# Kernel tuning notes

Measured on AMD Instinct MI355X. Metric: run time of the kernel, lower is better.

## Reference

```python
import jax, jax.numpy as jnp
import numpy as np

N_NODES = 100000
N_EDGES = 1600000
D_IN = 64
D_OUT = 64
EDGE_DIM = 16


def setup_inputs() -> dict:
    key = jax.random.key(0)
    ks = jax.random.split(key, 6)
    x = jax.random.normal(ks[0], (N_NODES, D_IN), dtype=jnp.float32)
    edge_index = jax.random.randint(ks[1], (2, N_EDGES), 0, N_NODES, dtype=jnp.int64)
    edge_feature = jax.random.normal(ks[2], (N_EDGES, EDGE_DIM), dtype=jnp.float32)
    W_edge = jax.random.normal(ks[3], (EDGE_DIM, 1), dtype=jnp.float32) * (1.0 / np.sqrt(EDGE_DIM))
    b_edge = jnp.zeros((1,), dtype=jnp.float32)
    W_node = jax.random.normal(ks[4], (D_OUT, D_IN), dtype=jnp.float32) * (1.0 / np.sqrt(D_IN))
    b_node = jnp.zeros((D_OUT,), dtype=jnp.float32)
    return {"x": x, "edge_index": edge_index, "edge_feature": edge_feature,
            "W_edge": W_edge, "b_edge": b_edge, "W_node": W_node, "b_node": b_node}


def reference(x, edge_index, edge_feature, W_edge, b_edge, W_node, b_node):
    # per-edge gate: Linear(edge_dim -> 1) + Sigmoid  -> [E]
    gate = jax.nn.sigmoid(edge_feature @ W_edge + b_edge)[:, 0]
    # node projection: Linear(in -> out)  -> [N, D_OUT]
    xp = x @ W_node.T + b_node
    row = edge_index[0]  # destination (SparseTensor row)
    col = edge_index[1]  # source gathered
    num_nodes = x.shape[0]
    # weighted gather of source node features  -> [E, D_OUT]
    msg = gate[:, None] * xp[col]
    summed = jax.ops.segment_sum(msg, row, num_segments=num_nodes)
    cnt = jax.ops.segment_sum(jnp.ones((row.shape[0],), dtype=xp.dtype), row,
                              num_segments=num_nodes)
    # reduce='mean': divide by row nnz count; empty rows stay 0
    out = summed / jnp.maximum(cnt, 1.0)[:, None]
    return out
```

## Files before the change

kernel.cpp:

```cpp
#include <hip/hip_runtime.h>
#include <math.h>

#define NN 100000
#define NE 1600000
#define DD 64
#define ED 16
#define BROWS 192
#define NBIN 521
#define NBIN_PAD 544
#define BCAP 3840
#define EPB 4096
#define NBLKA ((NE + EPB - 1) / EPB)


__device__ __forceinline__ unsigned short f2bf(float f) {
    unsigned int b = __float_as_uint(f);
    unsigned int r = (b + 0x7FFFu + ((b >> 16) & 1u)) >> 16;
    return (unsigned short)r;
}

__global__ __launch_bounds__(256) void proj_kernel(
    const float* __restrict__ x, const float* __restrict__ Wn,
    const float* __restrict__ bn, unsigned short* __restrict__ xpb,
    int* __restrict__ cursor) {
    __shared__ float4 xs[64 * 16];
    int tid = threadIdx.x;
    if (blockIdx.x == 0) {
        cursor[tid] = tid * BCAP;
        cursor[tid + 256] = (tid + 256) * BCAP;
        if (tid < NBIN_PAD - 512) cursor[tid + 512] = (tid + 512) * BCAP;
    }
    int o = tid & 63;
    int wave = tid >> 6;
    float4 Wr[16];
    const float4* Wn4 = reinterpret_cast<const float4*>(Wn);
#pragma unroll
    for (int k = 0; k < 16; ++k) Wr[k] = Wn4[o * 16 + k];
    float bo = bn[o];
    int n0 = blockIdx.x * 64;
    const float4* x4 = reinterpret_cast<const float4*>(x);
    long base = (long)n0 * 16;
    long limit = (long)NN * 16;
#pragma unroll
    for (int i = 0; i < 4; ++i) {
        long idx = base + tid + 256 * i;
        xs[tid + 256 * i] = (idx < limit) ? x4[idx] : make_float4(0.f, 0.f, 0.f, 0.f);
    }
    __syncthreads();
#pragma unroll
    for (int j = 0; j < 16; ++j) {
        int ln = wave * 16 + j;
        int n = n0 + ln;
        if (n >= NN) break;
        float acc = bo;
#pragma unroll
        for (int k = 0; k < 16; ++k) {
            float4 a = xs[ln * 16 + k];
            acc += a.x * Wr[k].x + a.y * Wr[k].y + a.z * Wr[k].z + a.w * Wr[k].w;
        }
        xpb[(long)n * DD + o] = f2bf(acc);
    }
}

__global__ __launch_bounds__(1024) void binA_kernel(
    const int* __restrict__ ei, const float* __restrict__ ef,
    const float* __restrict__ We, const float* __restrict__ be,
    int* __restrict__ cursor, int2* __restrict__ binned) {
    __shared__ int cnt[NBIN_PAD];
    __shared__ int base[NBIN_PAD];
    int tid = threadIdx.x;
    int e0 = blockIdx.x * EPB;
    if (tid < NBIN_PAD) cnt[tid] = 0;
    __syncthreads();
    int rows[4], cols[4];
#pragma unroll
    for (int i = 0; i < 4; ++i) {
        int e = e0 + tid + 1024 * i;
        bool ok = e < NE;
        rows[i] = ok ? ei[e] : -1;
        cols[i] = ok ? ei[NE + e] : 0;
        if (ok) atomicAdd(&cnt[rows[i] / BROWS], 1);
    }
    __syncthreads();
    if (tid < NBIN_PAD) {
        int c = cnt[tid];
        base[tid] = c ? atomicAdd(&cursor[tid], c) : 0;
    }
    __syncthreads();
    if (tid < NBIN_PAD) cnt[tid] = 0;
    __syncthreads();
    const float4* We4 = reinterpret_cast<const float4*>(We);
    float4 w0 = We4[0], w1 = We4[1], w2 = We4[2], w3 = We4[3];
    float bb = be[0];
#pragma unroll
    for (int i = 0; i < 4; ++i) {
        int e = e0 + tid + 1024 * i;
        if (e < NE) {
            const float4* ef4 = reinterpret_cast<const float4*>(ef + (size_t)e * ED);
            float4 a0 = ef4[0], a1 = ef4[1], a2 = ef4[2], a3 = ef4[3];
            float d = a0.x * w0.x + a0.y * w0.y + a0.z * w0.z + a0.w * w0.w
                    + a1.x * w1.x + a1.y * w1.y + a1.z * w1.z + a1.w * w1.w
                    + a2.x * w2.x + a2.y * w2.y + a2.z * w2.z + a2.w * w2.w
                    + a3.x * w3.x + a3.y * w3.y + a3.z * w3.z + a3.w * w3.w + bb;
            float g = 1.f / (1.f + expf(-d));
            int r = rows[i], c = cols[i];
            int bin = r / BROWS;
            int rl = r - bin * BROWS;
            int pos = base[bin] + atomicAdd(&cnt[bin], 1);
            binned[pos] = make_int2((rl << 24) | c, __float_as_int(g));
        }
    }
}

__global__ __launch_bounds__(512) void binB_kernel(
    const unsigned short* __restrict__ xpb, const int* __restrict__ cursor,
    const int2* __restrict__ binned, float* __restrict__ out) {
    __shared__ int2 sorted[BCAP];
    __shared__ int hist[256];
    __shared__ int offs[256];
    __shared__ int claim[BROWS];
    int tid = threadIdx.x;
    int b = blockIdx.x;
    if (tid < 256) { hist[tid] = 0; offs[tid] = 0; }
    if (tid < BROWS) claim[tid] = 0;
    __syncthreads();
    int bstart = b * BCAP;
    int nb = cursor[b] - bstart;
    for (int t = tid; t < nb; t += 512) {
        int w = binned[bstart + t].x;
        atomicAdd(&hist[(w >> 24) & 0xFF], 1);
    }
    __syncthreads();
    if (tid < 256) offs[tid] = hist[tid];
    __syncthreads();
    for (int d = 1; d < 256; d <<= 1) {
        int add = 0;
        if (tid < 256 && tid >= d) add = offs[tid - d];
        __syncthreads();
        if (tid < 256) offs[tid] += add;
        __syncthreads();
    }
    for (int t = tid; t < nb; t += 512) {
        int2 e = binned[bstart + t];
        int rl = (e.x >> 24) & 0xFF;
        int pos = offs[rl] - hist[rl] + atomicAdd(&claim[rl], 1);
        sorted[pos] = e;
    }
    __syncthreads();
    int lane = tid & 63;
    int wv = tid >> 6;
    int half = lane >> 5;
    int hl = lane & 31;
#pragma unroll 1
    for (int i = 0; i < 24; ++i) {
        int rl = wv + 8 * i;
        int row = b * BROWS + rl;
        if (row >= NN) break;
        int dn = hist[rl];
        int s0 = offs[rl] - dn;
        float ax = 0.f, ay = 0.f;
        for (int j = 0; j < dn; j += 16) {
#pragma unroll
            for (int k = 0; k < 8; ++k) {
                int ei_ = j + 2 * k + half;
                int2 e = sorted[s0 + min(ei_, dn - 1)];
                float g = (ei_ < dn) ? __int_as_float(e.y) : 0.f;
                int col = e.x & 0x1FFFF;
                unsigned int u = *reinterpret_cast<const unsigned int*>(
                    xpb + (size_t)col * DD + 2 * hl);
                ax += g * __uint_as_float((u & 0xFFFFu) << 16);
                ay += g * __uint_as_float(u & 0xFFFF0000u);
            }
        }
        ax += __shfl_xor(ax, 32);
        ay += __shfl_xor(ay, 32);
        if (half == 0) {
            float dv = fmaxf((float)dn, 1.f);
            reinterpret_cast<float2*>(out)[(size_t)row * 32 + hl] =
                make_float2(ax / dv, ay / dv);
        }
    }
}

extern "C" void kernel_launch(void* const* d_in, const int* in_sizes, int n_in,
                              void* d_out, int out_size, void* d_ws, size_t ws_size,
                              hipStream_t stream) {
    const float* x  = (const float*)d_in[0];
    const int*   ei = (const int*)d_in[1];
    const float* ef = (const float*)d_in[2];
    const float* We = (const float*)d_in[3];
    const float* be = (const float*)d_in[4];
    const float* Wn = (const float*)d_in[5];
    const float* bn = (const float*)d_in[6];
    float* out = (float*)d_out;

    unsigned short* xpb = (unsigned short*)d_ws;
    int*  cursor = (int*)d_ws + 3200000;
    int2* binned = (int2*)((int*)d_ws + 3200544);

    proj_kernel<<<(NN + 63) / 64, 256, 0, stream>>>(x, Wn, bn, xpb, cursor);
    binA_kernel<<<NBLKA, 1024, 0, stream>>>(ei, ef, We, be, cursor, binned);
    binB_kernel<<<NBIN, 512, 0, stream>>>(xpb, cursor, binned, out);
}
```

Before: 129.1 us.

## Split gate computation into separate kernel with 16-bit quantized gates, vectorize binning

Moves the per-edge sigmoid gate into its own kernel that writes a 16-bit fixed-point gate array. The binning kernel then reads only indices and the compact gates, using vectorized int4 loads over 8 edges per thread. It takes per-bin slots from the first shared atomic pass, which drops the second counting pass and one sync. This adds a kernel launch and an extra write and read of the gate array, and it lowers gate precision to 1/65535.

After: 127.0 us. Within noise of the previous version (-1.6%).

```diff
diff --git a/kernel.cpp b/kernel.cpp
--- a/kernel.cpp
+++ b/kernel.cpp
@@ -9,7 +9,7 @@
 #define NBIN 521
 #define NBIN_PAD 544
 #define BCAP 3840
-#define EPB 4096
+#define EPB 8192
 #define NBLKA ((NE + EPB - 1) / EPB)
 
 
@@ -62,53 +62,70 @@
     }
 }
 
+__global__ __launch_bounds__(256) void gate_kernel(
+    const float* __restrict__ ef, const float* __restrict__ We,
+    const float* __restrict__ be, unsigned short* __restrict__ g16) {
+    int e = blockIdx.x * 256 + threadIdx.x;
+    if (e >= NE) return;
+    const float4* ef4 = reinterpret_cast<const float4*>(ef + (size_t)e * ED);
+    const float4* We4 = reinterpret_cast<const float4*>(We);
+    float4 a0 = ef4[0], a1 = ef4[1], a2 = ef4[2], a3 = ef4[3];
+    float4 w0 = We4[0], w1 = We4[1], w2 = We4[2], w3 = We4[3];
+    float d = a0.x * w0.x + a0.y * w0.y + a0.z * w0.z + a0.w * w0.w
+            + a1.x * w1.x + a1.y * w1.y + a1.z * w1.z + a1.w * w1.w
+            + a2.x * w2.x + a2.y * w2.y + a2.z * w2.z + a2.w * w2.w
+            + a3.x * w3.x + a3.y * w3.y + a3.z * w3.z + a3.w * w3.w + be[0];
+    float g = 1.f / (1.f + expf(-d));
+    int q = (int)(g * 65535.f + 0.5f);
+    g16[e] = (unsigned short)min(q, 65535);
+}
+
 __global__ __launch_bounds__(1024) void binA_kernel(
-    const int* __restrict__ ei, const float* __restrict__ ef,
-    const float* __restrict__ We, const float* __restrict__ be,
+    const int* __restrict__ ei, const unsigned short* __restrict__ g16,
     int* __restrict__ cursor, int2* __restrict__ binned) {
     __shared__ int cnt[NBIN_PAD];
-    __shared__ int base[NBIN_PAD];
+    __shared__ int basev[NBIN_PAD];
     int tid = threadIdx.x;
     int e0 = blockIdx.x * EPB;
     if (tid < NBIN_PAD) cnt[tid] = 0;
     __syncthreads();
-    int rows[4], cols[4];
-#pragma unroll
-    for (int i = 0; i < 4; ++i) {
-        int e = e0 + tid + 1024 * i;
-        bool ok = e < NE;
-        rows[i] = ok ? ei[e] : -1;
-        cols[i] = ok ? ei[NE + e] : 0;
-        if (ok) atomicAdd(&cnt[rows[i] / BROWS], 1);
+    int e_base = e0 + tid * 8;
+    bool ok = e_base < NE;
+    int4 ra, rb, ca, cb;
+    ushort4 ga, gb;
+    int s0=0,s1=0,s2=0,s3=0,s4=0,s5=0,s6=0,s7=0;
+    int b0=0,b1=0,b2=0,b3=0,b4=0,b5=0,b6=0,b7=0;
+    if (ok) {
+        const int4* pr = reinterpret_cast<const int4*>(ei + e_base);
+        ra = pr[0]; rb = pr[1];
+        const int4* pc = reinterpret_cast<const int4*>(ei + NE + e_base);
+        ca = pc[0]; cb = pc[1];
+        const ushort4* pg = reinterpret_cast<const ushort4*>(g16 + e_base);
+        ga = pg[0]; gb = pg[1];
+        b0 = ra.x / BROWS; s0 = atomicAdd(&cnt[b0], 1);
+        b1 = ra.y / BROWS; s1 = atomicAdd(&cnt[b1], 1);
+        b2 = ra.z / BROWS; s2 = atomicAdd(&cnt[b2], 1);
+        b3 = ra.w / BROWS; s3 = atomicAdd(&cnt[b3], 1);
+        b4 = rb.x / BROWS; s4 = atomicAdd(&cnt[b4], 1);
+        b5 = rb.y / BROWS; s5 = atomicAdd(&cnt[b5], 1);
+        b6 = rb.z / BROWS; s6 = atomicAdd(&cnt[b6], 1);
+        b7 = rb.w / BROWS; s7 = atomicAdd(&cnt[b7], 1);
     }
     __syncthreads();
     if (tid < NBIN_PAD) {
         int c = cnt[tid];
-        base[tid] = c ? atomicAdd(&cursor[tid], c) : 0;
-    }
-    __syncthreads();
-    if (tid < NBIN_PAD) cnt[tid] = 0;
-    __syncthreads();
-    const float4* We4 = reinterpret_cast<const float4*>(We);
-    float4 w0 = We4[0], w1 = We4[1], w2 = We4[2], w3 = We4[3];
-    float bb = be[0];
-#pragma unroll
-    for (int i = 0; i < 4; ++i) {
-        int e = e0 + tid + 1024 * i;
-        if (e < NE) {
-            const float4* ef4 = reinterpret_cast<const float4*>(ef + (size_t)e * ED);
-            float4 a0 = ef4[0], a1 = ef4[1], a2 = ef4[2], a3 = ef4[3];
-            float d = a0.x * w0.x + a0.y * w0.y + a0.z * w0.z + a0.w * w0.w
-                    + a1.x * w1.x + a1.y * w1.y + a1.z * w1.z + a1.w * w1.w
-                    + a2.x * w2.x + a2.y * w2.y + a2.z * w2.z + a2.w * w2.w
-                    + a3.x * w3.x + a3.y * w3.y + a3.z * w3.z + a3.w * w3.w + bb;
-            float g = 1.f / (1.f + expf(-d));
-            int r = rows[i], c = cols[i];
-            int bin = r / BROWS;
-            int rl = r - bin * BROWS;
-            int pos = base[bin] + atomicAdd(&cnt[bin], 1);
-            binned[pos] = make_int2((rl << 24) | c, __float_as_int(g));
-        }
+        basev[tid] = c ? atomicAdd(&cursor[tid], c) : 0;
+    }
+    __syncthreads();
+    if (ok) {
+#define EMIT(BV, SV, RR, CC, GG) \
+        binned[basev[BV] + SV] = \
+            make_int2((((RR) - (BV) * BROWS) << 24) | (CC), (int)(GG));
+        EMIT(b0, s0, ra.x, ca.x, ga.x) EMIT(b1, s1, ra.y, ca.y, ga.y)
+        EMIT(b2, s2, ra.z, ca.z, ga.z) EMIT(b3, s3, ra.w, ca.w, ga.w)
+        EMIT(b4, s4, rb.x, cb.x, gb.x) EMIT(b5, s5, rb.y, cb.y, gb.y)
+        EMIT(b6, s6, rb.z, cb.z, gb.z) EMIT(b7, s7, rb.w, cb.w, gb.w)
+#undef EMIT
     }
 }
 
@@ -151,6 +168,7 @@
     int wv = tid >> 6;
     int half = lane >> 5;
     int hl = lane & 31;
+    const float gscale = 1.f / 65535.f;
 #pragma unroll 1
     for (int i = 0; i < 24; ++i) {
         int rl = wv + 8 * i;
@@ -164,7 +182,7 @@
             for (int k = 0; k < 8; ++k) {
                 int ei_ = j + 2 * k + half;
                 int2 e = sorted[s0 + min(ei_, dn - 1)];
-                float g = (ei_ < dn) ? __int_as_float(e.y) : 0.f;
+                float g = (ei_ < dn) ? (float)e.y * gscale : 0.f;
                 int col = e.x & 0x1FFFF;
                 unsigned int u = *reinterpret_cast<const unsigned int*>(
                     xpb + (size_t)col * DD + 2 * hl);
@@ -196,9 +214,11 @@
 
     unsigned short* xpb = (unsigned short*)d_ws;
     int*  cursor = (int*)d_ws + 3200000;
-    int2* binned = (int2*)((int*)d_ws + 3200544);
+    unsigned short* g16 = (unsigned short*)((int*)d_ws + 3200544);
+    int2* binned = (int2*)((int*)d_ws + 4000544);
 
     proj_kernel<<<(NN + 63) / 64, 256, 0, stream>>>(x, Wn, bn, xpb, cursor);
-    binA_kernel<<<NBLKA, 1024, 0, stream>>>(ei, ef, We, be, cursor, binned);
+    gate_kernel<<<(NE + 255) / 256, 256, 0, stream>>>(ef, We, be, g16);
+    binA_kernel<<<NBLKA, 1024, 0, stream>>>(ei, g16, cursor, binned);
     binB_kernel<<<NBIN, 512, 0, stream>>>(xpb, cursor, binned, out);
 }
```
